# Performance work log

Hardware: AMD Instinct MI355X
Metric: run time of the kernel (lower is better)

Reference implementation:

```python
import jax, jax.numpy as jnp
import numpy as np

B, S, D, H, HD, NF, NL, V = 16, 2048, 768, 12, 64, 32, 12, 2362
EPS = 1e-6  # fast_transformers LinearAttention eps


def _rope_tables(seq_len, dim):
    inv_freq = 1.0 / (10000.0 ** (jnp.arange(0, dim, 2, dtype=jnp.float32) / dim))
    t = jnp.arange(seq_len, dtype=jnp.float32)
    freqs = jnp.einsum('s,f->sf', t, inv_freq)
    emb = jnp.concatenate([freqs, freqs], axis=-1)[None, :, None, :]  # [1,S,1,HD]
    return jnp.cos(emb), jnp.sin(emb)


def _rot_half(x):
    x1, x2 = jnp.split(x, 2, axis=-1)
    return jnp.concatenate([-x2, x1], axis=-1)


def _ln(x, g, b):
    m = jnp.mean(x, axis=-1, keepdims=True)
    v = jnp.var(x, axis=-1, keepdims=True)
    return (x - m) / jnp.sqrt(v + 1e-5) * g + b


def setup_inputs():
    key = jax.random.key(0)
    ks = jax.random.split(key, 16)
    w = lambda k, shape: jax.random.normal(k, shape, jnp.float32) * 0.02
    return {
        'idx': jax.random.randint(ks[0], (B, S), 0, V),
        'mask': jnp.ones((B, S), jnp.int32),
        'emb': w(ks[1], (V, D)),
        'wq': w(ks[2], (NL, D, D)), 'bq': jnp.zeros((NL, D), jnp.float32),
        'wk': w(ks[3], (NL, D, D)), 'bk': jnp.zeros((NL, D), jnp.float32),
        'wv': w(ks[4], (NL, D, D)), 'bv': jnp.zeros((NL, D), jnp.float32),
        'wo': w(ks[5], (NL, D, D)), 'bo': jnp.zeros((NL, D), jnp.float32),
        'omega': jax.random.normal(ks[6], (NL, HD, NF), jnp.float32),
        'g1': jnp.ones((NL, D), jnp.float32), 'be1': jnp.zeros((NL, D), jnp.float32),
        'w1': w(ks[7], (NL, D, D)), 'c1': jnp.zeros((NL, D), jnp.float32),
        'w2': w(ks[8], (NL, D, D)), 'c2': jnp.zeros((NL, D), jnp.float32),
        'g2': jnp.ones((NL, D), jnp.float32), 'be2': jnp.zeros((NL, D), jnp.float32),
        'gf': jnp.ones((D,), jnp.float32), 'bf': jnp.zeros((D,), jnp.float32),
    }


def reference(idx, mask, emb, wq, bq, wk, bk, wv, bv, wo, bo, omega,
              g1, be1, w1, c1, w2, c2, g2, be2, gf, bf):
    x = emb[idx]                     # token embedding [B,S,D]; dropout = identity (eval)
    m = mask.astype(x.dtype)         # LengthMask from mask.sum(-1); mask is contiguous ones
    cos, sin = _rope_tables(S, HD)
    for l in range(NL):
        q = (x @ wq[l] + bq[l]).reshape(B, S, H, HD)
        k = (x @ wk[l] + bk[l]).reshape(B, S, H, HD)
        v = (x @ wv[l] + bv[l]).reshape(B, S, H, HD)
        q = q * cos + _rot_half(q) * sin
        k = k * cos + _rot_half(k) * sin
        # GeneralizedRandomFeatures: phi(x) = relu(x @ omega)
        Qf = jax.nn.relu(jnp.einsum('bshd,df->bshf', q, omega[l]))
        Kf = jax.nn.relu(jnp.einsum('bshd,df->bshf', k, omega[l])) * m[:, :, None, None]
        KV = jnp.einsum('bshf,bshd->bhfd', Kf, v)                       # [B,H,NF,HD]
        Z = 1.0 / (jnp.einsum('bshf,bhf->bsh', Qf, Kf.sum(axis=1)) + EPS)
        a = jnp.einsum('bshf,bhfd,bsh->bshd', Qf, KV, Z).reshape(B, S, D)
        x = x + (a @ wo[l] + bo[l])           # residual (dropout=identity)
        x = _ln(x, g1[l], be1[l])             # post-norm
        y = jax.nn.gelu(x @ w1[l] + c1[l], approximate=False) @ w2[l] + c2[l]
        x = _ln(x + y, g2[l], be2[l])
    return _ln(x, gf, bf)                     # final encoder LayerNorm
```

## Files before the change

### kernel.cpp

```cpp
#include <hip/hip_runtime.h>
#include <cstdint>
#include <cstddef>

typedef __bf16 bf16;
typedef __bf16 bf16x8 __attribute__((ext_vector_type(8)));
typedef __bf16 bf16x4 __attribute__((ext_vector_type(4)));
typedef float f32x4 __attribute__((ext_vector_type(4)));

#define NB 16
#define SS 2048
#define HH 12
#define NLL 12
#define MTOK (NB*SS)

#define BARRIER() do { asm volatile("" ::: "memory"); __builtin_amdgcn_s_barrier(); asm volatile("" ::: "memory"); } while (0)
#define VMCNT0()  asm volatile("s_waitcnt vmcnt(0)" ::: "memory")

__device__ __forceinline__ void load16_lds(const bf16* g, bf16* l) {
    __builtin_amdgcn_global_load_lds((const __attribute__((address_space(1))) void*)g,
                                     (__attribute__((address_space(3))) void*)l, 16, 0, 0);
}

__global__ void diag_k(float* out, float code) {
    if (threadIdx.x == 0 && blockIdx.x == 0) out[0] = code;
}

__global__ __launch_bounds__(256) void packw_k(const float* __restrict__ wq, const float* __restrict__ wk,
                                               const float* __restrict__ wv, const float* __restrict__ wo,
                                               const float* __restrict__ w1, const float* __restrict__ w2,
                                               int l, bf16* qkvT_l, bf16* oT_l, bf16* w1T_l, bf16* w2T_l) {
    __shared__ float tile[32][33];
    int which = blockIdx.z;
    const float* srcs[6] = {wq, wk, wv, wo, w1, w2};
    const float* src = srcs[which] + (size_t)l * 589824;
    bf16* dst;
    if (which < 3)       dst = qkvT_l + (size_t)which * 589824;
    else if (which == 3) dst = oT_l;
    else if (which == 4) dst = w1T_l;
    else                 dst = w2T_l;
    int tx = threadIdx.x, ty = threadIdx.y;
    int bx = blockIdx.x, by = blockIdx.y;
#pragma unroll
    for (int j = 0; j < 4; ++j)
        tile[ty + j*8][tx] = src[(size_t)(by*32 + ty + j*8) * 768 + bx*32 + tx];
    __syncthreads();
#pragma unroll
    for (int j = 0; j < 4; ++j)
        dst[(size_t)(bx*32 + ty + j*8) * 768 + by*32 + tx] = (bf16)tile[tx][ty + j*8];
}

__global__ void packb_k(const float* __restrict__ bq, const float* __restrict__ bk,
                        const float* __restrict__ bv, float* bqkv) {
    int i = blockIdx.x * 256 + threadIdx.x;
    if (i >= NLL * 2304) return;
    int l = i / 2304, c = i % 2304;
    float v = (c < 768) ? bq[l*768 + c] : (c < 1536) ? bk[l*768 + c - 768] : bv[l*768 + c - 1536];
    bqkv[i] = v;
}

__global__ void rope_k(float* cosT, float* sinT) {
    int i = blockIdx.x * 256 + threadIdx.x;
    int s = i >> 6, j = i & 63, f = j & 31;
    float inv = powf(10000.f, -(float)(2*f) * (1.0f/64.0f));
    float ang = (float)s * inv;
    cosT[i] = cosf(ang);
    sinT[i] = sinf(ang);
}

__global__ __launch_bounds__(192) void embed_k(const int* __restrict__ idx, const float* __restrict__ emb,
                                               float* __restrict__ x, bf16* __restrict__ xb) {
    size_t tok = blockIdx.x;
    int t = threadIdx.x;
    int id = idx[tok];
    float4 v = *(const float4*)&emb[(size_t)id * 768 + t*4];
    *(float4*)&x[tok * 768 + t*4] = v;
    bf16x4 o; o[0] = (bf16)v.x; o[1] = (bf16)v.y; o[2] = (bf16)v.z; o[3] = (bf16)v.w;
    *(bf16x4*)&xb[tok * 768 + t*4] = o;
}

template <int MODE>
__global__ __launch_bounds__(512, 2)
void gemm256_k(const bf16* __restrict__ A, const bf16* __restrict__ Bt,
               const float* __restrict__ bias, float* resout, bf16* outb, int N) {
    const int K = 768;
    __shared__ bf16 As[2][16384];
    __shared__ bf16 Bs[2][16384];
    const int t = threadIdx.x;
    const int w = t >> 6, lane = t & 63;
    const int wr = w >> 2, wc = w & 3;

    const int nx = gridDim.x;
    const int L = blockIdx.y * nx + blockIdx.x;
    const int xcd = L & 7, bi = L >> 3;
    const int bcol = (bi % nx) * 256;
    const int brow = ((bi / nx) * 8 + xcd) * 256;

    const int srow0 = t >> 3;
    const int scb   = (t & 7) * 16;
    const int scbs  = scb ^ ((srow0 & 7) << 4);
    const int scol  = scbs >> 1;

    auto stageA = [&](int s, int k0, int hh) {
        const bf16* g0 = A + (size_t)(brow + hh*128 + srow0)      * K + k0 + scol;
        const bf16* g1 = A + (size_t)(brow + hh*128 + srow0 + 64) * K + k0 + scol;
        load16_lds(g0, &As[s][hh*8192 + t*8]);
        load16_lds(g1, &As[s][hh*8192 + t*8 + 4096]);
    };
    auto stageB = [&](int s, int k0, int hh) {
        const bf16* g0 = Bt + (size_t)(bcol + hh*128 + srow0)      * K + k0 + scol;
        const bf16* g1 = Bt + (size_t)(bcol + hh*128 + srow0 + 64) * K + k0 + scol;
        load16_lds(g0, &Bs[s][hh*8192 + t*8]);
        load16_lds(g1, &Bs[s][hh*8192 + t*8 + 4096]);
    };

    const int rowa = lane & 15, kg = lane >> 4;
    const int rsw  = (rowa & 7) << 4;

    f32x4  acc[8][4] = {};
    bf16x8 af[4][2];
    bf16x8 bg[2][2][2];

#define LOADAF(CUR, MH)                                                          \
    _Pragma("unroll") for (int mi2 = 0; mi2 < 4; ++mi2)                          \
    _Pragma("unroll") for (int ks = 0; ks < 2; ++ks) {                           \
        int lrow = wr*128 + (MH)*64 + mi2*16 + rowa;                             \
        int cbyt = (ks*64 + kg*16) ^ rsw;                                        \
        af[mi2][ks] = *(const bf16x8*)&As[CUR][lrow*64 + (cbyt >> 1)];           \
    }
#define LOADBG(CUR, NH)                                                          \
    _Pragma("unroll") for (int ni2 = 0; ni2 < 2; ++ni2)                          \
    _Pragma("unroll") for (int ks = 0; ks < 2; ++ks) {                           \
        int lrow = wc*64 + (NH)*32 + ni2*16 + rowa;                              \
        int cbyt = (ks*64 + kg*16) ^ rsw;                                        \
        bg[NH][ni2][ks] = *(const bf16x8*)&Bs[CUR][lrow*64 + (cbyt >> 1)];       \
    }
#define MFMAQ(MH, NH)                                                            \
    __builtin_amdgcn_s_setprio(1);                                               \
    _Pragma("unroll") for (int mi2 = 0; mi2 < 4; ++mi2)                          \
    _Pragma("unroll") for (int ni2 = 0; ni2 < 2; ++ni2)                          \
    _Pragma("unroll") for (int ks = 0; ks < 2; ++ks)                             \
        acc[(MH)*4+mi2][(NH)*2+ni2] = __builtin_amdgcn_mfma_f32_16x16x32_bf16(   \
            af[mi2][ks], bg[NH][ni2][ks], acc[(MH)*4+mi2][(NH)*2+ni2], 0, 0, 0); \
    __builtin_amdgcn_s_setprio(0);

    stageA(0, 0, 0); stageA(0, 0, 1); stageB(0, 0, 0); stageB(0, 0, 1);
    VMCNT0();
    BARRIER();

    for (int kt = 0; kt < 12; ++kt) {
        const int cur = kt & 1, nb = cur ^ 1;
        const int kn = (kt + 1) * 64;
        const bool st = (kt < 11);
        LOADAF(cur, 0);
        LOADBG(cur, 0);
        if (st) { stageA(nb, kn, 0); stageA(nb, kn, 1); }
        BARRIER();
        MFMAQ(0, 0);
        BARRIER();
        LOADBG(cur, 1);
        if (st) stageB(nb, kn, 0);
        BARRIER();
        MFMAQ(0, 1);
        BARRIER();
        LOADAF(cur, 1);
        if (st) stageB(nb, kn, 1);
        BARRIER();
        MFMAQ(1, 1);
        BARRIER();
        MFMAQ(1, 0);
        VMCNT0();
        BARRIER();
    }
#undef LOADAF
#undef LOADBG
#undef MFMAQ

    const int r0 = (lane >> 4) * 4, c0 = lane & 15;
#pragma unroll
    for (int mi = 0; mi < 8; ++mi) {
#pragma unroll
        for (int ni = 0; ni < 4; ++ni) {
            int col = bcol + wc * 64 + ni * 16 + c0;
            float bv = bias[col];
#pragma unroll
            for (int r = 0; r < 4; ++r) {
                int row = brow + wr * 128 + mi * 16 + r0 + r;
                float v = acc[mi][ni][r] + bv;
                size_t o = (size_t)row * N + col;
                if (MODE == 0) outb[o] = (bf16)v;
                else if (MODE == 1) outb[o] = (bf16)(0.5f * v * (1.f + erff(v * 0.70710678118f)));
                else resout[o] = v + resout[o];
            }
        }
    }
}

template <int MODE>
__global__ __launch_bounds__(256)
void gemm128_k(const bf16* __restrict__ A, const bf16* __restrict__ Bt,
               const float* __restrict__ bias, float* resout, bf16* outb, int N) {
    const int K = 768;
    __shared__ bf16 As[128 * 64];
    __shared__ bf16 Bs[128 * 64];
    const int t = threadIdx.x;
    const int w = t >> 6, lane = t & 63;
    const int wr = w >> 1, wc = w & 1;

    const int nx = gridDim.x;
    const int L = blockIdx.y * nx + blockIdx.x;
    const int xcd = L & 7, bi = L >> 3;
    const int bcol = (bi % nx) * 128;
    const int brow = ((bi / nx) * 8 + xcd) * 128;

    const int srow = t >> 3;
    const int scol = (((t & 7) * 16) ^ ((srow & 7) << 4)) >> 1;
    const int rowa = lane & 15, kg = lane >> 4;
    const int rsw  = (rowa & 7) << 4;

    f32x4 acc[4][4] = {};

    for (int k0 = 0; k0 < K; k0 += 64) {
        __syncthreads();
#pragma unroll
        for (int j = 0; j < 4; ++j) {
            load16_lds(A  + (size_t)(brow + j*32 + srow) * K + k0 + scol, &As[j*2048 + t*8]);
            load16_lds(Bt + (size_t)(bcol + j*32 + srow) * K + k0 + scol, &Bs[j*2048 + t*8]);
        }
        __syncthreads();
        bf16x8 af[4][2], bg[4][2];
#pragma unroll
        for (int mi = 0; mi < 4; ++mi)
#pragma unroll
            for (int ks = 0; ks < 2; ++ks)
                af[mi][ks] = *(const bf16x8*)&As[(wr*64 + mi*16 + rowa)*64 + (((ks*64 + kg*16) ^ rsw) >> 1)];
#pragma unroll
        for (int ni = 0; ni < 4; ++ni)
#pragma unroll
            for (int ks = 0; ks < 2; ++ks)
                bg[ni][ks] = *(const bf16x8*)&Bs[(wc*64 + ni*16 + rowa)*64 + (((ks*64 + kg*16) ^ rsw) >> 1)];
#pragma unroll
        for (int mi = 0; mi < 4; ++mi)
#pragma unroll
            for (int ni = 0; ni < 4; ++ni)
#pragma unroll
                for (int ks = 0; ks < 2; ++ks)
                    acc[mi][ni] = __builtin_amdgcn_mfma_f32_16x16x32_bf16(af[mi][ks], bg[ni][ks], acc[mi][ni], 0, 0, 0);
    }

    const int r0 = (lane >> 4) * 4, c0 = lane & 15;
#pragma unroll
    for (int mi = 0; mi < 4; ++mi) {
#pragma unroll
        for (int ni = 0; ni < 4; ++ni) {
            int col = bcol + wc * 64 + ni * 16 + c0;
            float bv = bias[col];
#pragma unroll
            for (int r = 0; r < 4; ++r) {
                int row = brow + wr * 64 + mi * 16 + r0 + r;
                float v = acc[mi][ni][r] + bv;
                size_t o = (size_t)row * N + col;
                if (MODE == 0) outb[o] = (bf16)v;
                else if (MODE == 1) outb[o] = (bf16)(0.5f * v * (1.f + erff(v * 0.70710678118f)));
                else resout[o] = v + resout[o];
            }
        }
    }
}

__global__ __launch_bounds__(192) void phi_k(const bf16* __restrict__ qkv, const float* __restrict__ cosT,
                                             const float* __restrict__ sinT, const float* __restrict__ omega_l,
                                             const int* __restrict__ mask, bf16* __restrict__ Qf,
                                             bf16* __restrict__ Kf) {
    __shared__ float roped[2][4][12][65];
    __shared__ float om[64][32];
    int t = threadIdx.x;
    size_t tok0 = (size_t)blockIdx.x * 4;

    for (int i = t; i < 2048; i += 192) ((float*)om)[i] = omega_l[i];

    {
        int side = t / 96, cr = t % 96, h = cr >> 3, cq = cr & 7;
        float sgn = (cq < 4) ? -1.f : 1.f;
        for (int it = 0; it < 4; ++it) {
            size_t tokg = tok0 + it;
            int s = (int)(tokg & (SS - 1));
            const bf16* rowp = qkv + tokg * 2304 + side * 768 + h * 64;
            bf16x8 mv = *(const bf16x8*)(rowp + cq * 8);
            bf16x8 pv = *(const bf16x8*)(rowp + (cq ^ 4) * 8);
            const float* cp = cosT + s * 64 + cq * 8;
            const float* sp = sinT + s * 64 + cq * 8;
#pragma unroll
            for (int e = 0; e < 8; ++e) {
                float r = (float)mv[e] * cp[e] + sgn * (float)pv[e] * sp[e];
                roped[side][it][h][cq * 8 + e] = r;
            }
        }
    }
    __syncthreads();

    int side = t / 96, rr = t % 96, h = rr >> 3, f0 = (rr & 7) * 4;
    float acc[4][4] = {};
    for (int d = 0; d < 64; ++d) {
        float4 o = *(const float4*)&om[d][f0];
#pragma unroll
        for (int tk = 0; tk < 4; ++tk) {
            float qv = roped[side][tk][h][d];
            acc[tk][0] += qv * o.x; acc[tk][1] += qv * o.y;
            acc[tk][2] += qv * o.z; acc[tk][3] += qv * o.w;
        }
    }
    bf16* outb = (side == 0) ? Qf : Kf;
#pragma unroll
    for (int tk = 0; tk < 4; ++tk) {
        size_t tokg = tok0 + tk;
        float m = (side == 1) ? (float)mask[tokg] : 1.f;
        bf16x4 v;
        v[0] = (bf16)(fmaxf(acc[tk][0], 0.f) * m);
        v[1] = (bf16)(fmaxf(acc[tk][1], 0.f) * m);
        v[2] = (bf16)(fmaxf(acc[tk][2], 0.f) * m);
        v[3] = (bf16)(fmaxf(acc[tk][3], 0.f) * m);
        *(bf16x4*)&outb[(tokg * 12 + h) * 32 + f0] = v;
    }
}

__global__ __launch_bounds__(256) void kvp_k(const bf16* __restrict__ Kf, const bf16* __restrict__ qkv,
                                             float* __restrict__ KVp, float* __restrict__ Ksp) {
    int ch = blockIdx.x, h = blockIdx.y, b = blockIdx.z;
    __shared__ float kts[64][32];
    __shared__ bf16 vts[64][64];
    int t = threadIdx.x;
    int fg = t & 15, dg = t >> 4;
    int f0 = fg * 2, d0 = dg * 4;
    float acc[8] = {};
    float ksm[2] = {};
    for (int s0 = ch * 256; s0 < ch * 256 + 256; s0 += 64) {
        __syncthreads();
        {
            int row = t >> 2, slot = t & 3;
            bf16x8 k8 = *(const bf16x8*)&Kf[((size_t)(b * SS + s0 + row) * 12 + h) * 32 + slot * 8];
#pragma unroll
            for (int e = 0; e < 8; ++e) kts[row][slot * 8 + e] = (float)k8[e];
            int c0 = t, c1 = t + 256;
            *(float4*)&vts[c0 >> 3][(c0 & 7) * 8] =
                *(const float4*)&qkv[(size_t)(b * SS + s0 + (c0 >> 3)) * 2304 + 1536 + h * 64 + (c0 & 7) * 8];
            *(float4*)&vts[c1 >> 3][(c1 & 7) * 8] =
                *(const float4*)&qkv[(size_t)(b * SS + s0 + (c1 >> 3)) * 2304 + 1536 + h * 64 + (c1 & 7) * 8];
        }
        __syncthreads();
#pragma unroll 4
        for (int sl = 0; sl < 64; ++sl) {
            float2 kk = *(const float2*)&kts[sl][f0];
            bf16x4 vv = *(const bf16x4*)&vts[sl][d0];
            float v0 = (float)vv[0], v1 = (float)vv[1], v2 = (float)vv[2], v3 = (float)vv[3];
            acc[0] += kk.x * v0; acc[1] += kk.x * v1; acc[2] += kk.x * v2; acc[3] += kk.x * v3;
            acc[4] += kk.y * v0; acc[5] += kk.y * v1; acc[6] += kk.y * v2; acc[7] += kk.y * v3;
            if (dg == 0) { ksm[0] += kk.x; ksm[1] += kk.y; }
        }
    }
    size_t base = (((size_t)(b * 12 + h) * 8 + ch) * 32) * 64;
#pragma unroll
    for (int i = 0; i < 2; ++i)
#pragma unroll
        for (int j = 0; j < 4; ++j)
            KVp[base + (size_t)(f0 + i) * 64 + d0 + j] = acc[i * 4 + j];
    if (dg == 0) {
        size_t kb = ((size_t)(b * 12 + h) * 8 + ch) * 32;
        Ksp[kb + f0] = ksm[0]; Ksp[kb + f0 + 1] = ksm[1];
    }
}

__global__ __launch_bounds__(256) void kvc_k(const float* __restrict__ KVp, const float* __restrict__ Ksp,
                                             float* __restrict__ KV, float* __restrict__ Ksum) {
    int bh = blockIdx.x, t = threadIdx.x;
    size_t base = (size_t)bh * 8 * 2048;
    float v[8] = {};
    for (int ch = 0; ch < 8; ++ch)
#pragma unroll
        for (int j = 0; j < 8; ++j) v[j] += KVp[base + (size_t)ch * 2048 + t * 8 + j];
#pragma unroll
    for (int j = 0; j < 8; ++j) KV[(size_t)bh * 2048 + t * 8 + j] = v[j];
    if (t < 32) {
        float s = 0.f;
        for (int ch = 0; ch < 8; ++ch) s += Ksp[((size_t)bh * 8 + ch) * 32 + t];
        Ksum[(size_t)bh * 32 + t] = s;
    }
}

__global__ __launch_bounds__(256) void comb_k(const bf16* __restrict__ Qf, const float* __restrict__ KV,
                                              const float* __restrict__ Ksum, bf16* __restrict__ aout) {
    int ch = blockIdx.x, h = blockIdx.y, b = blockIdx.z;
    int bh = b * 12 + h;
    int t = threadIdx.x, sl = t >> 6, d = t & 63;
    const float* kvb = KV + (size_t)bh * 2048;
    const float* ksb = Ksum + (size_t)bh * 32;
    float kvcol[32], ksr[32];
#pragma unroll
    for (int f = 0; f < 32; ++f) kvcol[f] = kvb[f * 64 + d];
#pragma unroll
    for (int f = 0; f < 32; ++f) ksr[f] = ksb[f];
    for (int g = 0; g < 16; ++g) {
        int s = ch * 64 + g * 4 + sl;
        size_t tok = (size_t)b * SS + s;
        const bf16* qf = Qf + (tok * 12 + h) * 32;
        float accd = 0.f, accz = 0.f;
#pragma unroll
        for (int fb = 0; fb < 4; ++fb) {
            bf16x8 q8 = *(const bf16x8*)(qf + fb * 8);
#pragma unroll
            for (int e = 0; e < 8; ++e) {
                float q = (float)q8[e];
                accd += q * kvcol[fb * 8 + e];
                accz += q * ksr[fb * 8 + e];
            }
        }
        float z = 1.f / (accz + 1e-6f);
        aout[tok * 768 + h * 64 + d] = (bf16)(accd * z);
    }
}

__global__ __launch_bounds__(192) void ln_k(const float* src, const float* __restrict__ g,
                                            const float* __restrict__ be, float* xout,
                                            bf16* xbout) {
    size_t tok = blockIdx.x;
    int t = threadIdx.x;
    float4 v = *(const float4*)&src[tok * 768 + t * 4];
    float s = v.x + v.y + v.z + v.w;
    float q = v.x * v.x + v.y * v.y + v.z * v.z + v.w * v.w;
#pragma unroll
    for (int off = 32; off > 0; off >>= 1) { s += __shfl_down(s, off); q += __shfl_down(q, off); }
    __shared__ float sred[3], qred[3];
    int w = t >> 6, lane = t & 63;
    if (lane == 0) { sred[w] = s; qred[w] = q; }
    __syncthreads();
    s = sred[0] + sred[1] + sred[2];
    q = qred[0] + qred[1] + qred[2];
    float mean = s * (1.f / 768.f);
    float var = q * (1.f / 768.f) - mean * mean;
    float inv = rsqrtf(var + 1e-5f);
    float4 gg = *(const float4*)&g[t * 4];
    float4 bb = *(const float4*)&be[t * 4];
    float4 o;
    o.x = (v.x - mean) * inv * gg.x + bb.x;
    o.y = (v.y - mean) * inv * gg.y + bb.y;
    o.z = (v.z - mean) * inv * gg.z + bb.z;
    o.w = (v.w - mean) * inv * gg.w + bb.w;
    *(float4*)&xout[tok * 768 + t * 4] = o;
    if (xbout) {
        bf16x4 ob; ob[0] = (bf16)o.x; ob[1] = (bf16)o.y; ob[2] = (bf16)o.z; ob[3] = (bf16)o.w;
        *(bf16x4*)&xbout[tok * 768 + t * 4] = ob;
    }
}

extern "C" void kernel_launch(void* const* d_in, const int* in_sizes, int n_in,
                              void* d_out, int out_size, void* d_ws, size_t ws_size,
                              hipStream_t stream) {
    const int*   idx   = (const int*)d_in[0];
    const int*   mask  = (const int*)d_in[1];
    const float* emb   = (const float*)d_in[2];
    const float* wq    = (const float*)d_in[3];
    const float* bq    = (const float*)d_in[4];
    const float* wk    = (const float*)d_in[5];
    const float* bk    = (const float*)d_in[6];
    const float* wv    = (const float*)d_in[7];
    const float* bv    = (const float*)d_in[8];
    const float* wo    = (const float*)d_in[9];
    const float* bo    = (const float*)d_in[10];
    const float* omega = (const float*)d_in[11];
    const float* g1    = (const float*)d_in[12];
    const float* be1   = (const float*)d_in[13];
    const float* w1    = (const float*)d_in[14];
    const float* c1    = (const float*)d_in[15];
    const float* w2    = (const float*)d_in[16];
    const float* c2    = (const float*)d_in[17];
    const float* g2    = (const float*)d_in[18];
    const float* be2   = (const float*)d_in[19];
    const float* gf    = (const float*)d_in[20];
    const float* bff   = (const float*)d_in[21];
    float* dout = (float*)d_out;

    char* wsb = (char*)d_ws;
    size_t off = 0;
    auto nxt = [&](size_t bytes) -> void* {
        void* p = wsb + off;
        off += bytes;
        off = (off + 255) & ~(size_t)255;
        return p;
    };

    float* cosT  = (float*)nxt((size_t)SS * 64 * 4);
    float* sinT  = (float*)nxt((size_t)SS * 64 * 4);
    bf16*  qkvTl = (bf16*)nxt((size_t)2304 * 768 * 2);
    bf16*  oTl   = (bf16*)nxt((size_t)768 * 768 * 2);
    bf16*  w1Tl  = (bf16*)nxt((size_t)768 * 768 * 2);
    bf16*  w2Tl  = (bf16*)nxt((size_t)768 * 768 * 2);
    float* bqkv  = (float*)nxt((size_t)NLL * 2304 * 4);
    float* x     = (float*)nxt((size_t)MTOK * 768 * 4);
    bf16*  xb    = (bf16*)nxt((size_t)MTOK * 768 * 2);
    bf16*  qkv   = (bf16*)nxt((size_t)MTOK * 2304 * 2);
    bf16*  Qf    = (bf16*)nxt((size_t)MTOK * 384 * 2);
    bf16*  Kf    = (bf16*)nxt((size_t)MTOK * 384 * 2);
    float* KVp   = (float*)nxt((size_t)NB * HH * 8 * 2048 * 4);
    float* Ksp   = (float*)nxt((size_t)NB * HH * 8 * 32 * 4);
    float* KV    = (float*)nxt((size_t)NB * HH * 2048 * 4);
    float* Ksum  = (float*)nxt((size_t)NB * HH * 32 * 4);
    size_t needed = off;

    if (ws_size < needed) {
        diag_k<<<dim3(1), dim3(64), 0, stream>>>(dout, 10000.f + (float)(ws_size >> 20));
        return;
    }

    bf16* abuf = qkv;
    bf16* h1   = (bf16*)((char*)qkv + (size_t)MTOK * 768 * 2);

    packb_k<<<dim3((NLL * 2304 + 255) / 256), dim3(256), 0, stream>>>(bq, bk, bv, bqkv);
    rope_k<<<dim3(SS * 64 / 256), dim3(256), 0, stream>>>(cosT, sinT);
    embed_k<<<dim3(MTOK), dim3(192), 0, stream>>>(idx, emb, x, xb);

    for (int l = 0; l < NLL; ++l) {
        const float* bqkv_l = bqkv + (size_t)l * 2304;
        const float* om_l   = omega + (size_t)l * 2048;

        packw_k<<<dim3(24, 24, 6), dim3(32, 8), 0, stream>>>(wq, wk, wv, wo, w1, w2, l, qkvTl, oTl, w1Tl, w2Tl);
        gemm256_k<0><<<dim3(9, 128), dim3(512), 0, stream>>>(xb, qkvTl, bqkv_l, nullptr, qkv, 2304);
        phi_k<<<dim3(MTOK / 4), dim3(192), 0, stream>>>(qkv, cosT, sinT, om_l, mask, Qf, Kf);
        kvp_k<<<dim3(8, HH, NB), dim3(256), 0, stream>>>(Kf, qkv, KVp, Ksp);
        kvc_k<<<dim3(NB * HH), dim3(256), 0, stream>>>(KVp, Ksp, KV, Ksum);
        comb_k<<<dim3(32, HH, NB), dim3(256), 0, stream>>>(Qf, KV, Ksum, abuf);
        gemm128_k<2><<<dim3(6, 256), dim3(256), 0, stream>>>(abuf, oTl, bo + (size_t)l * 768, x, nullptr, 768);
        ln_k<<<dim3(MTOK), dim3(192), 0, stream>>>(x, g1 + (size_t)l * 768, be1 + (size_t)l * 768, x, xb);
        gemm128_k<1><<<dim3(6, 256), dim3(256), 0, stream>>>(xb, w1Tl, c1 + (size_t)l * 768, nullptr, h1, 768);
        gemm128_k<2><<<dim3(6, 256), dim3(256), 0, stream>>>(h1, w2Tl, c2 + (size_t)l * 768, x, nullptr, 768);
        ln_k<<<dim3(MTOK), dim3(192), 0, stream>>>(x, g2 + (size_t)l * 768, be2 + (size_t)l * 768, x, xb);
    }
    ln_k<<<dim3(MTOK), dim3(192), 0, stream>>>(x, gf, bff, dout, nullptr);
}
```

Measured before the change: 8.535 ms.

## Stage GEMM epilogues through LDS and fuse residual add into LayerNorm

```diff
diff --git a/kernel.cpp b/kernel.cpp
--- a/kernel.cpp
+++ b/kernel.cpp
@@ -78,10 +78,9 @@
     *(bf16x4*)&xb[tok * 768 + t*4] = o;
 }
 
-template <int MODE>
 __global__ __launch_bounds__(512, 2)
 void gemm256_k(const bf16* __restrict__ A, const bf16* __restrict__ Bt,
-               const float* __restrict__ bias, float* resout, bf16* outb, int N) {
+               const float* __restrict__ bias, bf16* __restrict__ outb, int N) {
     const int K = 768;
     __shared__ bf16 As[2][16384];
     __shared__ bf16 Bs[2][16384];
@@ -175,22 +174,32 @@
 #undef LOADBG
 #undef MFMAQ
 
+    bf16* Cs = &As[0][0];
     const int r0 = (lane >> 4) * 4, c0 = lane & 15;
-#pragma unroll
-    for (int mi = 0; mi < 8; ++mi) {
-#pragma unroll
-        for (int ni = 0; ni < 4; ++ni) {
-            int col = bcol + wc * 64 + ni * 16 + c0;
-            float bv = bias[col];
-#pragma unroll
-            for (int r = 0; r < 4; ++r) {
-                int row = brow + wr * 128 + mi * 16 + r0 + r;
-                float v = acc[mi][ni][r] + bv;
-                size_t o = (size_t)row * N + col;
-                if (MODE == 0) outb[o] = (bf16)v;
-                else if (MODE == 1) outb[o] = (bf16)(0.5f * v * (1.f + erff(v * 0.70710678118f)));
-                else resout[o] = v + resout[o];
-            }
+    const int ch = t & 15, rr = t >> 4;
+#pragma unroll
+    for (int h = 0; h < 2; ++h) {
+        __syncthreads();
+        if ((wc >> 1) == h) {
+            const int lc0 = (wc & 1) * 64;
+#pragma unroll
+            for (int mi = 0; mi < 8; ++mi)
+#pragma unroll
+                for (int ni = 0; ni < 4; ++ni) {
+                    int col = bcol + wc * 64 + ni * 16 + c0;
+                    float bv = bias[col];
+#pragma unroll
+                    for (int r = 0; r < 4; ++r)
+                        Cs[(wr*128 + mi*16 + r0 + r) * 128 + lc0 + ni*16 + c0] =
+                            (bf16)(acc[mi][ni][r] + bv);
+                }
+        }
+        __syncthreads();
+#pragma unroll
+        for (int i = 0; i < 8; ++i) {
+            int row = rr + i * 32;
+            *(bf16x8*)&outb[(size_t)(brow + row) * N + bcol + h*128 + ch*8] =
+                *(const bf16x8*)&Cs[row * 128 + ch * 8];
         }
     }
 }
@@ -198,10 +207,11 @@
 template <int MODE>
 __global__ __launch_bounds__(256)
 void gemm128_k(const bf16* __restrict__ A, const bf16* __restrict__ Bt,
-               const float* __restrict__ bias, float* resout, bf16* outb, int N) {
+               const float* __restrict__ bias, bf16* __restrict__ outb, int N) {
     const int K = 768;
-    __shared__ bf16 As[128 * 64];
-    __shared__ bf16 Bs[128 * 64];
+    __shared__ bf16 sh[16384];
+    bf16* As = sh;
+    bf16* Bs = sh + 8192;
     const int t = threadIdx.x;
     const int w = t >> 6, lane = t & 63;
     const int wr = w >> 1, wc = w & 1;
@@ -247,23 +257,28 @@
                     acc[mi][ni] = __builtin_amdgcn_mfma_f32_16x16x32_bf16(af[mi][ks], bg[ni][ks], acc[mi][ni], 0, 0, 0);
     }
 
+    __syncthreads();
     const int r0 = (lane >> 4) * 4, c0 = lane & 15;
 #pragma unroll
-    for (int mi = 0; mi < 4; ++mi) {
+    for (int mi = 0; mi < 4; ++mi)
 #pragma unroll
         for (int ni = 0; ni < 4; ++ni) {
             int col = bcol + wc * 64 + ni * 16 + c0;
             float bv = bias[col];
 #pragma unroll
             for (int r = 0; r < 4; ++r) {
-                int row = brow + wr * 64 + mi * 16 + r0 + r;
                 float v = acc[mi][ni][r] + bv;
-                size_t o = (size_t)row * N + col;
-                if (MODE == 0) outb[o] = (bf16)v;
-                else if (MODE == 1) outb[o] = (bf16)(0.5f * v * (1.f + erff(v * 0.70710678118f)));
-                else resout[o] = v + resout[o];
+                if (MODE == 1) v = 0.5f * v * (1.f + erff(v * 0.70710678118f));
+                sh[(wr*64 + mi*16 + r0 + r) * 128 + wc*64 + ni*16 + c0] = (bf16)v;
             }
         }
+    __syncthreads();
+    const int ch = t & 15, rr = t >> 4;
+#pragma unroll
+    for (int i = 0; i < 8; ++i) {
+        int row = rr + i * 16;
+        *(bf16x8*)&outb[(size_t)(brow + row) * N + bcol + ch*8] =
+            *(const bf16x8*)&sh[row * 128 + ch * 8];
     }
 }
 
@@ -418,12 +433,16 @@
     }
 }
 
-__global__ __launch_bounds__(192) void ln_k(const float* src, const float* __restrict__ g,
-                                            const float* __restrict__ be, float* xout,
-                                            bf16* xbout) {
+__global__ __launch_bounds__(192) void ln2_k(const float* xsrc, const bf16* ysrc,
+                                             const float* __restrict__ g, const float* __restrict__ be,
+                                             float* xout, bf16* xbout) {
     size_t tok = blockIdx.x;
     int t = threadIdx.x;
-    float4 v = *(const float4*)&src[tok * 768 + t * 4];
+    float4 v = *(const float4*)&xsrc[tok * 768 + t * 4];
+    if (ysrc) {
+        bf16x4 yv = *(const bf16x4*)&ysrc[tok * 768 + t * 4];
+        v.x += (float)yv[0]; v.y += (float)yv[1]; v.z += (float)yv[2]; v.w += (float)yv[3];
+    }
     float s = v.x + v.y + v.z + v.w;
     float q = v.x * v.x + v.y * v.y + v.z * v.z + v.w * v.w;
 #pragma unroll
@@ -512,6 +531,7 @@
 
     bf16* abuf = qkv;
     bf16* h1   = (bf16*)((char*)qkv + (size_t)MTOK * 768 * 2);
+    bf16* y    = (bf16*)((char*)qkv + (size_t)MTOK * 768 * 4);
 
     packb_k<<<dim3((NLL * 2304 + 255) / 256), dim3(256), 0, stream>>>(bq, bk, bv, bqkv);
     rope_k<<<dim3(SS * 64 / 256), dim3(256), 0, stream>>>(cosT, sinT);
@@ -522,16 +542,16 @@
         const float* om_l   = omega + (size_t)l * 2048;
 
         packw_k<<<dim3(24, 24, 6), dim3(32, 8), 0, stream>>>(wq, wk, wv, wo, w1, w2, l, qkvTl, oTl, w1Tl, w2Tl);
-        gemm256_k<0><<<dim3(9, 128), dim3(512), 0, stream>>>(xb, qkvTl, bqkv_l, nullptr, qkv, 2304);
+        gemm256_k<<<dim3(9, 128), dim3(512), 0, stream>>>(xb, qkvTl, bqkv_l, qkv, 2304);
         phi_k<<<dim3(MTOK / 4), dim3(192), 0, stream>>>(qkv, cosT, sinT, om_l, mask, Qf, Kf);
         kvp_k<<<dim3(8, HH, NB), dim3(256), 0, stream>>>(Kf, qkv, KVp, Ksp);
         kvc_k<<<dim3(NB * HH), dim3(256), 0, stream>>>(KVp, Ksp, KV, Ksum);
         comb_k<<<dim3(32, HH, NB), dim3(256), 0, stream>>>(Qf, KV, Ksum, abuf);
-        gemm128_k<2><<<dim3(6, 256), dim3(256), 0, stream>>>(abuf, oTl, bo + (size_t)l * 768, x, nullptr, 768);
-        ln_k<<<dim3(MTOK), dim3(192), 0, stream>>>(x, g1 + (size_t)l * 768, be1 + (size_t)l * 768, x, xb);
-        gemm128_k<1><<<dim3(6, 256), dim3(256), 0, stream>>>(xb, w1Tl, c1 + (size_t)l * 768, nullptr, h1, 768);
-        gemm128_k<2><<<dim3(6, 256), dim3(256), 0, stream>>>(h1, w2Tl, c2 + (size_t)l * 768, x, nullptr, 768);
-        ln_k<<<dim3(MTOK), dim3(192), 0, stream>>>(x, g2 + (size_t)l * 768, be2 + (size_t)l * 768, x, xb);
-    }
-    ln_k<<<dim3(MTOK), dim3(192), 0, stream>>>(x, gf, bff, dout, nullptr);
-}
+        gemm128_k<0><<<dim3(6, 256), dim3(256), 0, stream>>>(abuf, oTl, bo + (size_t)l * 768, y, 768);
+        ln2_k<<<dim3(MTOK), dim3(192), 0, stream>>>(x, y, g1 + (size_t)l * 768, be1 + (size_t)l * 768, x, xb);
+        gemm128_k<1><<<dim3(6, 256), dim3(256), 0, stream>>>(xb, w1Tl, c1 + (size_t)l * 768, h1, 768);
+        gemm128_k<0><<<dim3(6, 256), dim3(256), 0, stream>>>(h1, w2Tl, c2 + (size_t)l * 768, y, 768);
+        ln2_k<<<dim3(MTOK), dim3(192), 0, stream>>>(x, y, g2 + (size_t)l * 768, be2 + (size_t)l * 768, x, xb);
+    }
+    ln2_k<<<dim3(MTOK), dim3(192), 0, stream>>>(x, nullptr, gf, bff, dout, nullptr);
+}
```

New measurement: 7.265 ms. -14.9%, faster.
